# Optimization experiments

Hardware: AMD Instinct MI355X
Metric: run time of the kernel (lower is better)

## Reference

```python
import jax, jax.numpy as jnp
import numpy as np

M, N = 256, 65536          # matched masks, flattened pred-mask pixels (256x256)
BLOCK_AREA = 4.0           # (H_t*W_t)/N with target masks at 512x512
H_T = W_T = 512.0
NUM_MASKS = 256.0
MAX_ITERS = 20
TOL = 1e-7


def _eval_fS(z, lam, Kcol):
    p = jax.nn.sigmoid(z + lam)
    f = jnp.sum(p, axis=-1, keepdims=True) - Kcol
    s = jnp.sum(p * (1.0 - p), axis=-1, keepdims=True)
    return f, s


def _shift_core(z, K):
    # z: (M,1,N) logits, K: (M,1) target counts. Safeguarded Newton/bisection
    # so that sum(sigmoid(z + lam)) == K per row. (torch ref uses float64;
    # we stay in input dtype for jit/bf16 compatibility.)
    n = z.shape[-1]
    K = jnp.clip(K, 0.0, float(n))
    z_max = jnp.max(z, axis=-1, keepdims=True)
    z_min = jnp.min(z, axis=-1, keepdims=True)
    L = -20.0 - z_max
    U = 20.0 - z_min

    def _logit(x, eps=1e-6):
        x = jnp.clip(x, eps, 1.0 - eps)
        return jnp.log(x) - jnp.log1p(-x)

    p0_mean = jnp.mean(jax.nn.sigmoid(z), axis=-1)
    t_mean = K / n
    lam = (_logit(t_mean) - _logit(p0_mean))[..., None]
    lam = jnp.clip(lam, L, U)
    Kcol = K[..., None]
    f, S = _eval_fS(z, lam, Kcol)

    def body(_, carry):
        lam, f, S, L, U = carry
        done = jnp.abs(f) <= TOL
        newton = lam - f / (S + 1e-18)
        oob = (newton < L) | (newton > U)
        lam_try = jnp.where(oob | done, lam, newton)
        f_try, _ = _eval_fS(z, lam_try, Kcol)
        no_improve = (jnp.abs(f_try) > jnp.abs(f)) & (~oob) & (~done)
        mid = 0.5 * (L + U)
        lam_next = jnp.where(oob | no_improve, mid, lam_try)
        f_next, S_next = _eval_fS(z, lam_next, Kcol)
        go_upper = f_next > 0
        U = jnp.where(go_upper, lam_next, U)
        L = jnp.where(go_upper, L, lam_next)
        return lam_next, f_next, S_next, L, U

    lam, f, S, L, U = jax.lax.fori_loop(0, MAX_ITERS, body, (lam, f, S, L, U))
    lam = jnp.clip(lam, L, U)
    return z + lam


def setup_inputs() -> dict:
    key = jax.random.key(0)
    k1, k2 = jax.random.split(key)
    logits = jax.random.normal(k1, (M, N), dtype=jnp.float32) * 2.0
    pos_counts = jax.random.uniform(k2, (M, N), dtype=jnp.float32) * BLOCK_AREA
    return {"logits": logits, "pos_counts": pos_counts}


def reference(logits, pos_counts):
    n = logits.shape[1]
    K_high = jnp.sum(pos_counts, axis=1)                      # (M,)
    K_low = jnp.clip(K_high / BLOCK_AREA, 0.0, float(n))      # (M,)
    z_shift = _shift_core(logits[:, None, :], K_low[:, None])[:, 0, :]
    # block-weighted BCE with logits (numerically stable form)
    abs_z = jnp.abs(z_shift)
    max_z = jnp.maximum(z_shift, 0.0)
    logexp = jnp.log1p(jnp.exp(-abs_z))
    loss_block = BLOCK_AREA * max_z - z_shift * pos_counts + BLOCK_AREA * logexp
    loss_mask = jnp.sum(jnp.sum(loss_block, axis=1) / (H_T * W_T)) / NUM_MASKS
    # dice on area-matched probabilities
    probs = jax.nn.sigmoid(z_shift)
    inter = jnp.sum(probs * pos_counts, axis=1)
    pred_sum = BLOCK_AREA * jnp.sum(probs, axis=1)
    loss_dice = jnp.sum(1.0 - (2.0 * inter + 1.0) / (pred_sum + K_high + 1.0)) / NUM_MASKS
    return jnp.stack([loss_mask, loss_dice])
```

## Files before the change

### kernel.cpp

```cpp
#include <hip/hip_runtime.h>
#include <math.h>

#define NCOLS 65536
#define MROWS 256
#define NBINS 1024
#define CHUNKS 8
#define CELEMS (NCOLS / CHUNKS)
#define K1_TPB 256
#define K1_ITERS (CELEMS / 4 / K1_TPB)
#define ZLO 20.0f
#define INVW ((float)NBINS / (2.0f * ZLO))
#define PSCALE 8192.0f

__device__ __forceinline__ float waveReduceSum(float v) {
#pragma unroll
  for (int off = 32; off > 0; off >>= 1) v += __shfl_xor(v, off, 64);
  return v;
}

__global__ __launch_bounds__(K1_TPB) void hist_kernel(
    const float* __restrict__ logits, const float* __restrict__ pos,
    unsigned int* __restrict__ gcnt, int* __restrict__ gpbin,
    float* __restrict__ gpos, float* __restrict__ gzp) {
  __shared__ unsigned int cnt[NBINS];
  __shared__ int pbin[NBINS];
  __shared__ float red[8];
  const int blk = blockIdx.x;
  const int row = blk / CHUNKS, chunk = blk % CHUNKS;
  const int tid = threadIdx.x, wid = tid >> 6, lane = tid & 63;

  for (int b = tid; b < NBINS; b += K1_TPB) { cnt[b] = 0u; pbin[b] = 0; }
  __syncthreads();

  const float4* z4 = (const float4*)(logits + (size_t)row * NCOLS + (size_t)chunk * CELEMS);
  const float4* p4 = (const float4*)(pos + (size_t)row * NCOLS + (size_t)chunk * CELEMS);
  float s_pos = 0.0f, s_zp = 0.0f;
#pragma unroll
  for (int i = 0; i < K1_ITERS; ++i) {
    float4 zv = z4[i * K1_TPB + tid];
    float4 pv = p4[i * K1_TPB + tid];
    s_pos += (pv.x + pv.y) + (pv.z + pv.w);
    s_zp += zv.x * pv.x + zv.y * pv.y + zv.z * pv.z + zv.w * pv.w;
    float zz[4] = {zv.x, zv.y, zv.z, zv.w};
    float pp[4] = {pv.x, pv.y, pv.z, pv.w};
#pragma unroll
    for (int c = 0; c < 4; ++c) {
      int b = (int)((zz[c] + ZLO) * INVW);
      b = min(max(b, 0), NBINS - 1);
      atomicAdd(&cnt[b], 1u);
      atomicAdd(&pbin[b], __float2int_rn(pp[c] * PSCALE));
    }
  }
  __syncthreads();
  for (int b = tid; b < NBINS; b += K1_TPB) {
    gcnt[(size_t)blk * NBINS + b] = cnt[b];
    gpbin[(size_t)blk * NBINS + b] = pbin[b];
  }
  s_pos = waveReduceSum(s_pos);
  s_zp = waveReduceSum(s_zp);
  if (lane == 0) { red[wid] = s_pos; red[4 + wid] = s_zp; }
  __syncthreads();
  if (tid == 0) {
    gpos[blk] = (red[0] + red[1]) + (red[2] + red[3]);
    gzp[blk] = (red[4] + red[5]) + (red[6] + red[7]);
  }
}

#define K2_TPB 256
#define BPT (NBINS / K2_TPB)

__global__ __launch_bounds__(K2_TPB) void solve_kernel(
    const unsigned int* __restrict__ gcnt, const int* __restrict__ gpbin,
    const float* __restrict__ gpos, const float* __restrict__ gzp,
    float* __restrict__ rowout) {
  __shared__ float red[12];
  const int row = blockIdx.x;
  const int tid = threadIdx.x, wid = tid >> 6, lane = tid & 63;

  float cntf[BPT], pbf[BPT], zc[BPT];
#pragma unroll
  for (int j = 0; j < BPT; ++j) {
    const int b = tid + j * K2_TPB;
    unsigned int c = 0u; int pq = 0;
    for (int ch = 0; ch < CHUNKS; ++ch) {
      const size_t base = (size_t)(row * CHUNKS + ch) * NBINS + b;
      c += gcnt[base];
      pq += gpbin[base];
    }
    cntf[j] = (float)c;
    pbf[j] = (float)pq * (1.0f / PSCALE);
    zc[j] = -ZLO + ((float)b + 0.5f) / INVW;
  }
  float Kh = 0.0f, Szp = 0.0f;
  for (int ch = 0; ch < CHUNKS; ++ch) {
    Kh += gpos[row * CHUNKS + ch];
    Szp += gzp[row * CHUNKS + ch];
  }
  const float K = fminf(fmaxf(Kh * 0.25f, 0.0f), (float)NCOLS);

  float Lb = -2.0f * ZLO, Ub = 2.0f * ZLO, lam = 0.0f;
  for (int it = 0; it < 30; ++it) {
    float fp = 0.0f, sp = 0.0f;
#pragma unroll
    for (int j = 0; j < BPT; ++j) {
      float p = 1.0f / (1.0f + __expf(-(zc[j] + lam)));
      fp += cntf[j] * p;
      sp += cntf[j] * p * (1.0f - p);
    }
    fp = waveReduceSum(fp);
    sp = waveReduceSum(sp);
    __syncthreads();
    if (lane == 0) { red[wid] = fp; red[4 + wid] = sp; }
    __syncthreads();
    const float F = (red[0] + red[1]) + (red[2] + red[3]);
    const float S = (red[4] + red[5]) + (red[6] + red[7]);
    const float f = F - K;
    if (fabsf(f) <= 1e-2f) break;
    if (f > 0.0f) Ub = lam; else Lb = lam;
    const float newton = lam - f / (S + 1e-12f);
    lam = (newton > Lb && newton < Ub) ? newton : 0.5f * (Lb + Ub);
  }

  float tl = 0.0f, ti = 0.0f, tp = 0.0f;
#pragma unroll
  for (int j = 0; j < BPT; ++j) {
    const float zs = zc[j] + lam;
    const float e = __expf(-fabsf(zs));
    const float lg = __logf(1.0f + e);
    const float mz = fmaxf(zs, 0.0f);
    const float sig = (zs >= 0.0f) ? (1.0f / (1.0f + e)) : (e / (1.0f + e));
    tl += cntf[j] * (mz + lg);
    ti += pbf[j] * sig;
    tp += cntf[j] * sig;
  }
  tl = waveReduceSum(tl);
  ti = waveReduceSum(ti);
  tp = waveReduceSum(tp);
  __syncthreads();
  if (lane == 0) { red[wid] = tl; red[4 + wid] = ti; red[8 + wid] = tp; }
  __syncthreads();
  if (tid == 0) {
    const float loss = 4.0f * ((red[0] + red[1]) + (red[2] + red[3])) - (Szp + lam * Kh);
    float* o = rowout + row * 4;
    o[0] = loss;
    o[1] = (red[4] + red[5]) + (red[6] + red[7]);
    o[2] = (red[8] + red[9]) + (red[10] + red[11]);
    o[3] = Kh;
  }
}

__global__ void final_kernel(const float* __restrict__ rowout, float* __restrict__ out) {
  const int t = threadIdx.x;
  const float loss = rowout[t * 4 + 0];
  const float inter = rowout[t * 4 + 1];
  const float psum = rowout[t * 4 + 2];
  const float Kh = rowout[t * 4 + 3];
  float maskc = loss * (1.0f / (512.0f * 512.0f));
  float dicec = 1.0f - (2.0f * inter + 1.0f) / (4.0f * psum + Kh + 1.0f);
  maskc = waveReduceSum(maskc);
  dicec = waveReduceSum(dicec);
  __shared__ float red[8];
  const int wid = t >> 6, lane = t & 63;
  if (lane == 0) { red[wid] = maskc; red[4 + wid] = dicec; }
  __syncthreads();
  if (t == 0) {
    float a = 0.0f, b = 0.0f;
    for (int j = 0; j < 4; ++j) { a += red[j]; b += red[4 + j]; }
    out[0] = a / 256.0f;
    out[1] = b / 256.0f;
  }
}

#define FB_TPB 1024
#define FB_NV4 (NCOLS / 4 / FB_TPB)
__device__ __forceinline__ void fbReduce2(float a, float b, float* red,
                                          int wid, int lane, float& A, float& B) {
  a = waveReduceSum(a);
  b = waveReduceSum(b);
  __syncthreads();
  if (lane == 0) { red[wid] = a; red[16 + wid] = b; }
  __syncthreads();
  float ta = 0.0f, tb = 0.0f;
#pragma unroll
  for (int j = 0; j < 16; ++j) { ta += red[j]; tb += red[16 + j]; }
  A = ta; B = tb;
}

__global__ __launch_bounds__(FB_TPB) void fb_row_kernel(
    const float* __restrict__ logits, const float* __restrict__ pos,
    float* __restrict__ rowout) {
  __shared__ unsigned int h_cnt[2048];
  __shared__ int h_sum[2048];
  __shared__ float red[64];
  const int row = blockIdx.x;
  const int tid = threadIdx.x, wid = tid >> 6, lane = tid & 63;
  const float4* z4 = (const float4*)(logits + (size_t)row * NCOLS);
  const float4* p4 = (const float4*)(pos + (size_t)row * NCOLS);
  for (int b = tid; b < 2048; b += FB_TPB) { h_cnt[b] = 0u; h_sum[b] = 0; }
  __syncthreads();
  const float invw = 2048.0f / 40.0f;
  float s_pos = 0.0f;
#pragma unroll
  for (int i = 0; i < FB_NV4; ++i) {
    float4 zv = z4[i * FB_TPB + tid];
    float4 pv = p4[i * FB_TPB + tid];
    s_pos += (pv.x + pv.y) + (pv.z + pv.w);
    float zz[4] = {zv.x, zv.y, zv.z, zv.w};
#pragma unroll
    for (int c = 0; c < 4; ++c) {
      int b = (int)((zz[c] + 20.0f) * invw);
      b = min(max(b, 0), 2047);
      atomicAdd(&h_cnt[b], 1u);
      atomicAdd(&h_sum[b], __float2int_rn(zz[c] * 1024.0f));
    }
  }
  float K_high, dummy;
  fbReduce2(s_pos, 0.0f, red, wid, lane, K_high, dummy);
  float K = fminf(fmaxf(K_high * 0.25f, 0.0f), (float)NCOLS);
  const float c0 = (float)h_cnt[tid];
  const float c1 = (float)h_cnt[tid + FB_TPB];
  const float zb0 = (c0 > 0.0f) ? (float)h_sum[tid] / (1024.0f * c0) : 0.0f;
  const float zb1 = (c1 > 0.0f) ? (float)h_sum[tid + FB_TPB] / (1024.0f * c1) : 0.0f;
  float Lb = -40.0f, Ub = 40.0f, lam = 0.0f;
  for (int it = 0; it < 40; ++it) {
    float p0 = 1.0f / (1.0f + __expf(-(zb0 + lam)));
    float p1 = 1.0f / (1.0f + __expf(-(zb1 + lam)));
    float F, S;
    fbReduce2(c0 * p0 + c1 * p1, c0 * p0 * (1.0f - p0) + c1 * p1 * (1.0f - p1),
              red, wid, lane, F, S);
    float f = F - K;
    if (fabsf(f) <= 1e-3f) break;
    if (f > 0.0f) Ub = lam; else Lb = lam;
    float newton = lam - f / (S + 1e-12f);
    lam = (newton > Lb && newton < Ub) ? newton : 0.5f * (Lb + Ub);
  }
  float loss = 0.0f, inter = 0.0f, psum = 0.0f;
#pragma unroll
  for (int i = 0; i < FB_NV4; ++i) {
    float4 zv = z4[i * FB_TPB + tid];
    float4 pv = p4[i * FB_TPB + tid];
    float zz[4] = {zv.x, zv.y, zv.z, zv.w};
    float pp[4] = {pv.x, pv.y, pv.z, pv.w};
#pragma unroll
    for (int c = 0; c < 4; ++c) {
      float zs = zz[c] + lam;
      float q = __expf(-fabsf(zs));
      loss += 4.0f * fmaxf(zs, 0.0f) - zs * pp[c] + 4.0f * __logf(1.0f + q);
      float sig = (zs >= 0.0f) ? (1.0f / (1.0f + q)) : (q / (1.0f + q));
      inter += sig * pp[c];
      psum += sig;
    }
  }
  float TL, TI;
  fbReduce2(loss, inter, red, wid, lane, TL, TI);
  float TP, d2;
  fbReduce2(psum, 0.0f, red, wid, lane, TP, d2);
  if (tid == 0) {
    float* o = rowout + row * 4;
    o[0] = TL; o[1] = TI; o[2] = TP; o[3] = K_high;
  }
}

extern "C" void kernel_launch(void* const* d_in, const int* in_sizes, int n_in,
                              void* d_out, int out_size, void* d_ws, size_t ws_size,
                              hipStream_t stream) {
  const float* logits = (const float*)d_in[0];
  const float* pos = (const float*)d_in[1];
  char* ws = (char*)d_ws;

  const size_t nblk = (size_t)MROWS * CHUNKS;
  const size_t off_gcnt = 0;
  const size_t off_gpbin = off_gcnt + nblk * NBINS * sizeof(unsigned int);
  const size_t off_gpos = off_gpbin + nblk * NBINS * sizeof(int);
  const size_t off_gzp = off_gpos + nblk * sizeof(float);
  const size_t off_rowout = off_gzp + nblk * sizeof(float);
  const size_t needed = off_rowout + (size_t)MROWS * 4 * sizeof(float);

  if (ws_size >= needed) {
    unsigned int* gcnt = (unsigned int*)(ws + off_gcnt);
    int* gpbin = (int*)(ws + off_gpbin);
    float* gpos = (float*)(ws + off_gpos);
    float* gzp = (float*)(ws + off_gzp);
    float* rowout = (float*)(ws + off_rowout);
    hist_kernel<<<(int)nblk, K1_TPB, 0, stream>>>(logits, pos, gcnt, gpbin, gpos, gzp);
    solve_kernel<<<MROWS, K2_TPB, 0, stream>>>(gcnt, gpbin, gpos, gzp, rowout);
    final_kernel<<<1, 256, 0, stream>>>(rowout, (float*)d_out);
  } else {
    float* rowout = (float*)d_ws;
    fb_row_kernel<<<MROWS, FB_TPB, 0, stream>>>(logits, pos, rowout);
    final_kernel<<<1, 256, 0, stream>>>(rowout, (float*)d_out);
  }
}
```

Before: 38.44 us.

## Pack histogram count and pos into one 64-bit atomic, halve bins, single-wave solve

The histogram kernel now packs the per-bin count (upper bits) and the quantized pos sum (lower 40 bits) into one 64-bit shared-memory atomic, so each element costs one atomic instead of two. The bin count drops from 1024 to 512, and the loads are software-pipelined through register double-buffering. The solve kernel merges the chunks into shared memory and then runs the Newton/bisection loop in a single wavefront, which removes the block-level barriers on every iteration. The coarser bins add approximation error to the solved shift, and the iteration cap is raised to 40.

```diff
diff --git a/kernel.cpp b/kernel.cpp
--- a/kernel.cpp
+++ b/kernel.cpp
@@ -3,14 +3,17 @@
 
 #define NCOLS 65536
 #define MROWS 256
-#define NBINS 1024
+#define NBINS 512
 #define CHUNKS 8
 #define CELEMS (NCOLS / CHUNKS)
 #define K1_TPB 256
 #define K1_ITERS (CELEMS / 4 / K1_TPB)
 #define ZLO 20.0f
 #define INVW ((float)NBINS / (2.0f * ZLO))
+#define BINW (2.0f * ZLO / (float)NBINS)
 #define PSCALE 8192.0f
+#define CNT_SHIFT 40
+#define POS_MASK ((1ull << CNT_SHIFT) - 1ull)
 
 __device__ __forceinline__ float waveReduceSum(float v) {
 #pragma unroll
@@ -18,44 +21,69 @@
   return v;
 }
 
-__global__ __launch_bounds__(K1_TPB) void hist_kernel(
+__global__ __launch_bounds__(K1_TPB, 8) void hist_kernel(
     const float* __restrict__ logits, const float* __restrict__ pos,
-    unsigned int* __restrict__ gcnt, int* __restrict__ gpbin,
+    unsigned long long* __restrict__ gh,
     float* __restrict__ gpos, float* __restrict__ gzp) {
-  __shared__ unsigned int cnt[NBINS];
-  __shared__ int pbin[NBINS];
+  __shared__ unsigned long long h[NBINS];
   __shared__ float red[8];
   const int blk = blockIdx.x;
   const int row = blk / CHUNKS, chunk = blk % CHUNKS;
   const int tid = threadIdx.x, wid = tid >> 6, lane = tid & 63;
 
-  for (int b = tid; b < NBINS; b += K1_TPB) { cnt[b] = 0u; pbin[b] = 0; }
+#pragma unroll
+  for (int b = tid; b < NBINS; b += K1_TPB) h[b] = 0ull;
   __syncthreads();
 
   const float4* z4 = (const float4*)(logits + (size_t)row * NCOLS + (size_t)chunk * CELEMS);
   const float4* p4 = (const float4*)(pos + (size_t)row * NCOLS + (size_t)chunk * CELEMS);
   float s_pos = 0.0f, s_zp = 0.0f;
-#pragma unroll
-  for (int i = 0; i < K1_ITERS; ++i) {
-    float4 zv = z4[i * K1_TPB + tid];
-    float4 pv = p4[i * K1_TPB + tid];
-    s_pos += (pv.x + pv.y) + (pv.z + pv.w);
-    s_zp += zv.x * pv.x + zv.y * pv.y + zv.z * pv.z + zv.w * pv.w;
+
+  float4 zr[4], pr[4];
+#pragma unroll
+  for (int i = 0; i < 4; ++i) {
+    zr[i] = z4[i * K1_TPB + tid];
+    pr[i] = p4[i * K1_TPB + tid];
+  }
+#pragma unroll
+  for (int i = 0; i < 4; ++i) {
+    float4 zv = zr[i], pv = pr[i];
+    zr[i] = z4[(i + 4) * K1_TPB + tid];
+    pr[i] = p4[(i + 4) * K1_TPB + tid];
     float zz[4] = {zv.x, zv.y, zv.z, zv.w};
     float pp[4] = {pv.x, pv.y, pv.z, pv.w};
+    s_pos += (pp[0] + pp[1]) + (pp[2] + pp[3]);
+    s_zp += zz[0] * pp[0] + zz[1] * pp[1] + zz[2] * pp[2] + zz[3] * pp[3];
 #pragma unroll
     for (int c = 0; c < 4; ++c) {
       int b = (int)((zz[c] + ZLO) * INVW);
       b = min(max(b, 0), NBINS - 1);
-      atomicAdd(&cnt[b], 1u);
-      atomicAdd(&pbin[b], __float2int_rn(pp[c] * PSCALE));
-    }
-  }
-  __syncthreads();
-  for (int b = tid; b < NBINS; b += K1_TPB) {
-    gcnt[(size_t)blk * NBINS + b] = cnt[b];
-    gpbin[(size_t)blk * NBINS + b] = pbin[b];
-  }
+      unsigned long long pk = (1ull << CNT_SHIFT) |
+                              (unsigned long long)__float2int_rn(pp[c] * PSCALE);
+      atomicAdd(&h[b], pk);
+    }
+  }
+#pragma unroll
+  for (int i = 0; i < 4; ++i) {
+    float4 zv = zr[i], pv = pr[i];
+    float zz[4] = {zv.x, zv.y, zv.z, zv.w};
+    float pp[4] = {pv.x, pv.y, pv.z, pv.w};
+    s_pos += (pp[0] + pp[1]) + (pp[2] + pp[3]);
+    s_zp += zz[0] * pp[0] + zz[1] * pp[1] + zz[2] * pp[2] + zz[3] * pp[3];
+#pragma unroll
+    for (int c = 0; c < 4; ++c) {
+      int b = (int)((zz[c] + ZLO) * INVW);
+      b = min(max(b, 0), NBINS - 1);
+      unsigned long long pk = (1ull << CNT_SHIFT) |
+                              (unsigned long long)__float2int_rn(pp[c] * PSCALE);
+      atomicAdd(&h[b], pk);
+    }
+  }
+  __syncthreads();
+#pragma unroll
+  for (int b = tid; b < NBINS; b += K1_TPB)
+    gh[(size_t)blk * NBINS + b] = h[b];
+
   s_pos = waveReduceSum(s_pos);
   s_zp = waveReduceSum(s_zp);
   if (lane == 0) { red[wid] = s_pos; red[4 + wid] = s_zp; }
@@ -67,84 +95,81 @@
 }
 
 #define K2_TPB 256
-#define BPT (NBINS / K2_TPB)
 
 __global__ __launch_bounds__(K2_TPB) void solve_kernel(
-    const unsigned int* __restrict__ gcnt, const int* __restrict__ gpbin,
+    const unsigned long long* __restrict__ gh,
     const float* __restrict__ gpos, const float* __restrict__ gzp,
     float* __restrict__ rowout) {
-  __shared__ float red[12];
+  __shared__ unsigned long long hm[NBINS];
   const int row = blockIdx.x;
-  const int tid = threadIdx.x, wid = tid >> 6, lane = tid & 63;
-
-  float cntf[BPT], pbf[BPT], zc[BPT];
-#pragma unroll
-  for (int j = 0; j < BPT; ++j) {
+  const int tid = threadIdx.x;
+
+#pragma unroll
+  for (int j = 0; j < NBINS / K2_TPB; ++j) {
     const int b = tid + j * K2_TPB;
-    unsigned int c = 0u; int pq = 0;
-    for (int ch = 0; ch < CHUNKS; ++ch) {
-      const size_t base = (size_t)(row * CHUNKS + ch) * NBINS + b;
-      c += gcnt[base];
-      pq += gpbin[base];
-    }
-    cntf[j] = (float)c;
-    pbf[j] = (float)pq * (1.0f / PSCALE);
-    zc[j] = -ZLO + ((float)b + 0.5f) / INVW;
-  }
-  float Kh = 0.0f, Szp = 0.0f;
-  for (int ch = 0; ch < CHUNKS; ++ch) {
-    Kh += gpos[row * CHUNKS + ch];
-    Szp += gzp[row * CHUNKS + ch];
-  }
+    unsigned long long s = 0ull;
+#pragma unroll
+    for (int ch = 0; ch < CHUNKS; ++ch)
+      s += gh[(size_t)(row * CHUNKS + ch) * NBINS + b];
+    hm[b] = s;
+  }
+  __syncthreads();
+  if (tid >= 64) return;
+
+  const int lane = tid;
+  float cnt[8], pb[8], zc[8];
+#pragma unroll
+  for (int j = 0; j < 8; ++j) {
+    const int b = lane + 64 * j;
+    const unsigned long long v = hm[b];
+    cnt[j] = (float)(unsigned int)(v >> CNT_SHIFT);
+    pb[j] = (float)(unsigned long long)(v & POS_MASK) * (1.0f / PSCALE);
+    zc[j] = -ZLO + ((float)b + 0.5f) * BINW;
+  }
+  float Kh = (lane < CHUNKS) ? gpos[row * CHUNKS + lane] : 0.0f;
+  float Szp = (lane < CHUNKS) ? gzp[row * CHUNKS + lane] : 0.0f;
+  Kh = waveReduceSum(Kh);
+  Szp = waveReduceSum(Szp);
   const float K = fminf(fmaxf(Kh * 0.25f, 0.0f), (float)NCOLS);
 
   float Lb = -2.0f * ZLO, Ub = 2.0f * ZLO, lam = 0.0f;
-  for (int it = 0; it < 30; ++it) {
+  for (int it = 0; it < 40; ++it) {
     float fp = 0.0f, sp = 0.0f;
 #pragma unroll
-    for (int j = 0; j < BPT; ++j) {
-      float p = 1.0f / (1.0f + __expf(-(zc[j] + lam)));
-      fp += cntf[j] * p;
-      sp += cntf[j] * p * (1.0f - p);
+    for (int j = 0; j < 8; ++j) {
+      const float p = 1.0f / (1.0f + __expf(-(zc[j] + lam)));
+      fp += cnt[j] * p;
+      sp += cnt[j] * p * (1.0f - p);
     }
     fp = waveReduceSum(fp);
     sp = waveReduceSum(sp);
-    __syncthreads();
-    if (lane == 0) { red[wid] = fp; red[4 + wid] = sp; }
-    __syncthreads();
-    const float F = (red[0] + red[1]) + (red[2] + red[3]);
-    const float S = (red[4] + red[5]) + (red[6] + red[7]);
-    const float f = F - K;
+    const float f = fp - K;
     if (fabsf(f) <= 1e-2f) break;
     if (f > 0.0f) Ub = lam; else Lb = lam;
-    const float newton = lam - f / (S + 1e-12f);
+    const float newton = lam - f / (sp + 1e-12f);
     lam = (newton > Lb && newton < Ub) ? newton : 0.5f * (Lb + Ub);
   }
 
   float tl = 0.0f, ti = 0.0f, tp = 0.0f;
 #pragma unroll
-  for (int j = 0; j < BPT; ++j) {
+  for (int j = 0; j < 8; ++j) {
     const float zs = zc[j] + lam;
     const float e = __expf(-fabsf(zs));
     const float lg = __logf(1.0f + e);
     const float mz = fmaxf(zs, 0.0f);
     const float sig = (zs >= 0.0f) ? (1.0f / (1.0f + e)) : (e / (1.0f + e));
-    tl += cntf[j] * (mz + lg);
-    ti += pbf[j] * sig;
-    tp += cntf[j] * sig;
+    tl += cnt[j] * (mz + lg);
+    ti += pb[j] * sig;
+    tp += cnt[j] * sig;
   }
   tl = waveReduceSum(tl);
   ti = waveReduceSum(ti);
   tp = waveReduceSum(tp);
-  __syncthreads();
-  if (lane == 0) { red[wid] = tl; red[4 + wid] = ti; red[8 + wid] = tp; }
-  __syncthreads();
-  if (tid == 0) {
-    const float loss = 4.0f * ((red[0] + red[1]) + (red[2] + red[3])) - (Szp + lam * Kh);
+  if (lane == 0) {
     float* o = rowout + row * 4;
-    o[0] = loss;
-    o[1] = (red[4] + red[5]) + (red[6] + red[7]);
-    o[2] = (red[8] + red[9]) + (red[10] + red[11]);
+    o[0] = 4.0f * tl - (Szp + lam * Kh);
+    o[1] = ti;
+    o[2] = tp;
     o[3] = Kh;
   }
 }
@@ -269,21 +294,19 @@
   char* ws = (char*)d_ws;
 
   const size_t nblk = (size_t)MROWS * CHUNKS;
-  const size_t off_gcnt = 0;
-  const size_t off_gpbin = off_gcnt + nblk * NBINS * sizeof(unsigned int);
-  const size_t off_gpos = off_gpbin + nblk * NBINS * sizeof(int);
+  const size_t off_gh = 0;
+  const size_t off_gpos = off_gh + nblk * NBINS * sizeof(unsigned long long);
   const size_t off_gzp = off_gpos + nblk * sizeof(float);
   const size_t off_rowout = off_gzp + nblk * sizeof(float);
   const size_t needed = off_rowout + (size_t)MROWS * 4 * sizeof(float);
 
   if (ws_size >= needed) {
-    unsigned int* gcnt = (unsigned int*)(ws + off_gcnt);
-    int* gpbin = (int*)(ws + off_gpbin);
+    unsigned long long* gh = (unsigned long long*)(ws + off_gh);
     float* gpos = (float*)(ws + off_gpos);
     float* gzp = (float*)(ws + off_gzp);
     float* rowout = (float*)(ws + off_rowout);
-    hist_kernel<<<(int)nblk, K1_TPB, 0, stream>>>(logits, pos, gcnt, gpbin, gpos, gzp);
-    solve_kernel<<<MROWS, K2_TPB, 0, stream>>>(gcnt, gpbin, gpos, gzp, rowout);
+    hist_kernel<<<(int)nblk, K1_TPB, 0, stream>>>(logits, pos, gh, gpos, gzp);
+    solve_kernel<<<MROWS, K2_TPB, 0, stream>>>(gh, gpos, gzp, rowout);
     final_kernel<<<1, 256, 0, stream>>>(rowout, (float*)d_out);
   } else {
     float* rowout = (float*)d_ws;
```

Result: slower. 46.76 us (+21.7%).
